# Kernel tuning notes

Measured on AMD Instinct MI355X. Metric: run time of the kernel, lower is better.

## Reference

```python
import jax, jax.numpy as jnp
import numpy as np

B, T, DM = 2, 2048, 1024
H, HKV, DH = 16, 4, 64          # n_heads, n_kv_heads, head_dim
LAT, DFF = 64, 4096             # MLA latent dim, SwiGLU hidden (4*d_model)
SCALE = DH ** -0.5
ROPE_BASE = 10000.0


def _rope(x):
    # x: [B, T, h, DH]; split-half rotary
    half = DH // 2
    pos = jnp.arange(T, dtype=jnp.float32)
    inv_freq = 1.0 / (ROPE_BASE ** (jnp.arange(half, dtype=jnp.float32) / half))
    ang = pos[:, None] * inv_freq                      # [T, half]
    cos = jnp.cos(ang)[None, :, None, :]
    sin = jnp.sin(ang)[None, :, None, :]
    x1, x2 = x[..., :half], x[..., half:]
    return jnp.concatenate([x1 * cos - x2 * sin, x2 * cos + x1 * sin], axis=-1)


def setup_inputs() -> dict:
    key = jax.random.key(0)
    ks = jax.random.split(key, 9)
    init = lambda k, shape, fan: jax.random.normal(k, shape, jnp.float32) * (fan ** -0.5)
    return {
        "x": jax.random.normal(ks[0], (B, T, DM), jnp.float32),
        "Wq": init(ks[1], (DM, DM), DM),
        "Wkv_down": init(ks[2], (DM, LAT), DM),
        "Wk_up": init(ks[3], (LAT, HKV * DH), LAT),
        "Wv_up": init(ks[4], (LAT, HKV * DH), LAT),
        "Wgate": init(ks[5], (DH, DH), DH),
        "bgate": jnp.zeros((DH,), jnp.float32),
        "Wo1": init(ks[6], (DM, DFF), DM),
        "Wo2": init(ks[7], (DFF, DM), DFF),
    }


def reference(x, Wq, Wkv_down, Wk_up, Wv_up, Wgate, bgate, Wo1, Wo2):
    # GQA projections; MLA: shared low-rank latent -> K/V up-projections
    q = (x @ Wq).reshape(B, T, H, DH)
    lat = x @ Wkv_down                                  # [B, T, LAT]
    k = (lat @ Wk_up).reshape(B, T, HKV, DH)
    v = (lat @ Wv_up).reshape(B, T, HKV, DH)

    q = _rope(q)
    k = _rope(k)

    # repeat KV heads (GQA): kv head g serves q heads [g*rep, (g+1)*rep)
    rep = H // HKV
    k = jnp.repeat(k, rep, axis=2)                      # [B, T, H, DH]
    v = jnp.repeat(v, rep, axis=2)

    scores = jnp.einsum("bthd,bshd->bhts", q, k) * SCALE
    causal = jnp.tril(jnp.ones((T, T), dtype=bool))
    scores = jnp.where(causal[None, None], scores, -jnp.inf)
    attn = jax.nn.softmax(scores, axis=-1)
    out = jnp.einsum("bhts,bshd->bthd", attn, v)        # [B, T, H, DH]

    # Gated attention (G1, per_head): sigmoid gate after attention
    gate = jax.nn.sigmoid(out @ Wgate + bgate)
    out = (out * gate).reshape(B, T, DM)

    # SwiGLU-style out_proj: Linear -> SiLU -> Linear
    h = jax.nn.silu(out @ Wo1)
    return h @ Wo2
```

## Files before the change

kernel.cpp:

```cpp
#include <hip/hip_runtime.h>
#include <math.h>

#define NB 2
#define NT 2048
#define NDM 1024
#define NH 16
#define NHKV 4
#define NDH 64
#define NLAT 64
#define NDFF 4096

typedef __attribute__((ext_vector_type(4))) float fx4;
typedef __attribute__((ext_vector_type(8))) short bf8;
typedef __attribute__((ext_vector_type(4))) unsigned short us4;
typedef __attribute__((ext_vector_type(8))) unsigned short us8;

__device__ __forceinline__ unsigned short f2bf(float f) {
  union { float f; unsigned int u; } v; v.f = f;
  unsigned int u = v.u;
  u += 0x7fffu + ((u >> 16) & 1u);
  return (unsigned short)(u >> 16);
}
__device__ __forceinline__ float bf2f(unsigned short h) {
  union { unsigned u; float f; } v; v.u = ((unsigned)h) << 16; return v.f;
}

__global__ void conv_bf_k(const float* __restrict__ in,
                          unsigned short* __restrict__ out, int n8) {
  int idx = blockIdx.x * 256 + threadIdx.x;
  if (idx >= n8) return;
  fx4 a = *(const fx4*)(in + (size_t)idx * 8);
  fx4 b = *(const fx4*)(in + (size_t)idx * 8 + 4);
  us8 o = { f2bf(a[0]), f2bf(a[1]), f2bf(a[2]), f2bf(a[3]),
            f2bf(b[0]), f2bf(b[1]), f2bf(b[2]), f2bf(b[3]) };
  *(us8*)(out + (size_t)idx * 8) = o;
}

__global__ __launch_bounds__(256) void convT_bf_k(const float* __restrict__ W,
                                                  unsigned short* __restrict__ Wt,
                                                  int K, int N) {
  __shared__ float tile[64 * 65];
  const int t = threadIdx.x;
  const int k0 = blockIdx.x * 64, n0 = blockIdx.y * 64;
#pragma unroll
  for (int i = 0; i < 4; ++i) {
    int id = t + 256 * i;
    int row = id >> 4, c = (id & 15) * 4;
    fx4 v = *(const fx4*)(W + (size_t)(k0 + row) * N + n0 + c);
    tile[row * 65 + c + 0] = v[0];
    tile[row * 65 + c + 1] = v[1];
    tile[row * 65 + c + 2] = v[2];
    tile[row * 65 + c + 3] = v[3];
  }
  __syncthreads();
  const int nr = t >> 2, kc = (t & 3) * 16;
  us8 o0, o1;
#pragma unroll
  for (int e = 0; e < 8; ++e) o0[e] = f2bf(tile[(kc + e) * 65 + nr]);
#pragma unroll
  for (int e = 0; e < 8; ++e) o1[e] = f2bf(tile[(kc + 8 + e) * 65 + nr]);
  *(us8*)(Wt + (size_t)(n0 + nr) * K + k0 + kc) = o0;
  *(us8*)(Wt + (size_t)(n0 + nr) * K + k0 + kc + 8) = o1;
}

__device__ __forceinline__ bf8 fragG(const unsigned short* base, int row, int gr) {
  const unsigned short* rb = base + row * 64;
  const int r7 = row & 7;
  us4 lo = *(const us4*)(rb + 8 * ((gr >> 1) ^ r7) + 4 * (gr & 1));
  us4 hi = *(const us4*)(rb + 8 * (((gr + 4) >> 1) ^ r7) + 4 * (gr & 1));
  bf8 f;
  f[0] = (short)lo[0]; f[1] = (short)lo[1]; f[2] = (short)lo[2]; f[3] = (short)lo[3];
  f[4] = (short)hi[0]; f[5] = (short)hi[1]; f[6] = (short)hi[2]; f[7] = (short)hi[3];
  return f;
}

template<int EPI>
__global__ __launch_bounds__(256) void gemm_bf_k(const unsigned short* __restrict__ A,
                                                 const unsigned short* __restrict__ Bt,
                                                 void* __restrict__ Cp,
                                                 int M, int N, int K) {
  __shared__ __align__(16) unsigned short As[128 * 64];
  __shared__ __align__(16) unsigned short Bs[128 * 64];
  const int t = threadIdx.x;
  const int m0 = blockIdx.x * 128, n0 = blockIdx.y * 128;
  const int lane = t & 63, w = t >> 6;
  const int n = lane & 15, g = lane >> 4;
  const int wr = w >> 1, wc = w & 1;
  const int lrow = lane >> 3;
  const int lslot = (lane & 7) ^ lrow;
  const unsigned short* srcA = A  + (size_t)(m0 + 32 * w + lrow) * K + 8 * lslot;
  const unsigned short* srcB = Bt + (size_t)(n0 + 32 * w + lrow) * K + 8 * lslot;
  fx4 acc[4][4];
#pragma unroll
  for (int mt = 0; mt < 4; ++mt)
#pragma unroll
    for (int nt = 0; nt < 4; ++nt) acc[mt][nt] = fx4{0.f, 0.f, 0.f, 0.f};

  for (int k0 = 0; k0 < K; k0 += 64) {
    __syncthreads();
#pragma unroll
    for (int u = 0; u < 4; ++u) {
      __builtin_amdgcn_global_load_lds(
          (const __attribute__((address_space(1))) unsigned int*)(srcA + (size_t)(8 * u) * K + k0),
          (__attribute__((address_space(3))) unsigned int*)(As + (32 * w + 8 * u) * 64),
          16, 0, 0);
      __builtin_amdgcn_global_load_lds(
          (const __attribute__((address_space(1))) unsigned int*)(srcB + (size_t)(8 * u) * K + k0),
          (__attribute__((address_space(3))) unsigned int*)(Bs + (32 * w + 8 * u) * 64),
          16, 0, 0);
    }
    __syncthreads();
#pragma unroll
    for (int ks = 0; ks < 2; ++ks) {
      bf8 af[4], bfr[4];
#pragma unroll
      for (int mt = 0; mt < 4; ++mt)
        af[mt] = fragG(As, wr * 64 + mt * 16 + n, 8 * ks + g);
#pragma unroll
      for (int nt = 0; nt < 4; ++nt)
        bfr[nt] = fragG(Bs, wc * 64 + nt * 16 + n, 8 * ks + g);
#pragma unroll
      for (int mt = 0; mt < 4; ++mt)
#pragma unroll
        for (int nt = 0; nt < 4; ++nt)
          acc[mt][nt] = __builtin_amdgcn_mfma_f32_16x16x32_bf16(af[mt], bfr[nt], acc[mt][nt], 0, 0, 0);
    }
  }
#pragma unroll
  for (int mt = 0; mt < 4; ++mt)
#pragma unroll
    for (int nt = 0; nt < 4; ++nt)
#pragma unroll
      for (int r = 0; r < 4; ++r) {
        int row = m0 + wr * 64 + mt * 16 + 4 * g + r;
        int col = n0 + wc * 64 + nt * 16 + n;
        float v = acc[mt][nt][r];
        if (EPI == 1) {
          float s = v / (1.f + __expf(-v));
          ((unsigned short*)Cp)[(size_t)row * N + col] = f2bf(s);
        } else {
          ((float*)Cp)[(size_t)row * N + col] = v;
        }
      }
}

template<int ABF16, int EPI>
__global__ __launch_bounds__(256) void gemm_k(const void* __restrict__ Ap,
                                              const float* __restrict__ Bp,
                                              void* __restrict__ Cp,
                                              int M, int N, int K) {
  constexpr int LDK = 68;
  __shared__ unsigned short As[64 * LDK];
  __shared__ unsigned short Bs[64 * LDK];
  const int t = threadIdx.x;
  const int m0 = blockIdx.x * 64, n0 = blockIdx.y * 64;
  const int lane = t & 63, w = t >> 6;
  const int m16 = lane & 15, g = lane >> 4;
  const int arow = w * 16 + m16;
  fx4 acc[4] = {{0.f,0.f,0.f,0.f},{0.f,0.f,0.f,0.f},{0.f,0.f,0.f,0.f},{0.f,0.f,0.f,0.f}};

  for (int k0 = 0; k0 < K; k0 += 64) {
    __syncthreads();
#pragma unroll
    for (int i = 0; i < 4; ++i) {
      int id = t * 4 + i;
      int row = id >> 4, cg = (id & 15) * 4;
      if (ABF16) {
        const unsigned short* A = (const unsigned short*)Ap;
        *(us4*)(As + row * LDK + cg) =
            *(const us4*)(A + (size_t)(m0 + row) * K + k0 + cg);
      } else {
        const float* A = (const float*)Ap;
        fx4 a = *(const fx4*)(A + (size_t)(m0 + row) * K + k0 + cg);
        us4 ab = { f2bf(a[0]), f2bf(a[1]), f2bf(a[2]), f2bf(a[3]) };
        *(us4*)(As + row * LDK + cg) = ab;
      }
      fx4 bv = *(const fx4*)(Bp + (size_t)(k0 + row) * N + n0 + cg);
      Bs[(cg + 0) * LDK + row] = f2bf(bv[0]);
      Bs[(cg + 1) * LDK + row] = f2bf(bv[1]);
      Bs[(cg + 2) * LDK + row] = f2bf(bv[2]);
      Bs[(cg + 3) * LDK + row] = f2bf(bv[3]);
    }
    __syncthreads();
#pragma unroll
    for (int ks = 0; ks < 2; ++ks) {
      const int kb = ks * 32;
      us4 a0 = *(const us4*)(As + arow * LDK + kb + 4 * g);
      us4 a1 = *(const us4*)(As + arow * LDK + kb + 16 + 4 * g);
      bf8 af;
      af[0] = (short)a0[0]; af[1] = (short)a0[1]; af[2] = (short)a0[2]; af[3] = (short)a0[3];
      af[4] = (short)a1[0]; af[5] = (short)a1[1]; af[6] = (short)a1[2]; af[7] = (short)a1[3];
#pragma unroll
      for (int nt = 0; nt < 4; ++nt) {
        const int brow = nt * 16 + m16;
        us4 b0 = *(const us4*)(Bs + brow * LDK + kb + 4 * g);
        us4 b1 = *(const us4*)(Bs + brow * LDK + kb + 16 + 4 * g);
        bf8 bf_;
        bf_[0] = (short)b0[0]; bf_[1] = (short)b0[1]; bf_[2] = (short)b0[2]; bf_[3] = (short)b0[3];
        bf_[4] = (short)b1[0]; bf_[5] = (short)b1[1]; bf_[6] = (short)b1[2]; bf_[7] = (short)b1[3];
        acc[nt] = __builtin_amdgcn_mfma_f32_16x16x32_bf16(af, bf_, acc[nt], 0, 0, 0);
      }
    }
  }
#pragma unroll
  for (int nt = 0; nt < 4; ++nt) {
#pragma unroll
    for (int r = 0; r < 4; ++r) {
      int row = m0 + w * 16 + 4 * g + r;
      int col = n0 + nt * 16 + m16;
      float vv = acc[nt][r];
      if (EPI == 1) {
        float s = vv / (1.f + __expf(-vv));
        ((unsigned short*)Cp)[(size_t)row * N + col] = f2bf(s);
      } else {
        ((float*)Cp)[(size_t)row * N + col] = vv;
      }
    }
  }
}

__global__ void rope_k(float* __restrict__ x, int nheads, int total) {
  int idx = blockIdx.x * 256 + threadIdx.x;
  if (idx >= total) return;
  int i = idx & 31;
  int rest = idx >> 5;
  int tpos = (rest / nheads) % NT;
  float* p = x + (size_t)rest * NDH;
  float ang = (float)tpos * powf(10000.0f, -(float)i * (1.0f / 32.0f));
  float sn, cs;
  sincosf(ang, &sn, &cs);
  float x1 = p[i], x2 = p[i + 32];
  p[i]      = x1 * cs - x2 * sn;
  p[i + 32] = x2 * cs + x1 * sn;
}

__device__ __forceinline__ bf8 frag64(const unsigned short* base, int row, int gr) {
  const unsigned short* rb = base + row * 72;
  us4 lo = *(const us4*)(rb + 4 * gr);
  us4 hi = *(const us4*)(rb + 4 * gr + 16);
  bf8 f;
  f[0] = (short)lo[0]; f[1] = (short)lo[1]; f[2] = (short)lo[2]; f[3] = (short)lo[3];
  f[4] = (short)hi[0]; f[5] = (short)hi[1]; f[6] = (short)hi[2]; f[7] = (short)hi[3];
  return f;
}
__device__ __forceinline__ bf8 frag64v(const unsigned short* base, int row, int gr) {
  const unsigned short* rb = base + row * 72 + 8 * ((row >> 3) & 1);
  us4 lo = *(const us4*)(rb + 4 * gr);
  us4 hi = *(const us4*)(rb + 4 * gr + 16);
  bf8 f;
  f[0] = (short)lo[0]; f[1] = (short)lo[1]; f[2] = (short)lo[2]; f[3] = (short)lo[3];
  f[4] = (short)hi[0]; f[5] = (short)hi[1]; f[6] = (short)hi[2]; f[7] = (short)hi[3];
  return f;
}

__global__ __launch_bounds__(256) void attn_mfma_k(const float* __restrict__ qb,
                                                   const float* __restrict__ kb,
                                                   const float* __restrict__ vb,
                                                   const float* __restrict__ Wg,
                                                   const float* __restrict__ bg,
                                                   unsigned short* __restrict__ outp) {
  __shared__ __align__(16) char smem[36352];
  unsigned short* Qs  = (unsigned short*)smem;
  unsigned short* Ks  = Qs + 64 * 72;
  unsigned short* Vt  = Ks + 64 * 72;
  unsigned short* wgs = Vt + 64 * 72;
  float* outs = (float*)smem;

  const int t = threadIdx.x;
  const int q0 = blockIdx.x * 64;
  const int bh = blockIdx.y;
  const int b = bh >> 4, h = bh & 15, kvh = h >> 2;
  const int lane = t & 63, wq = t >> 6;
  const int n = lane & 15, g = lane >> 4;
  const int srow = 4 * wq + g;
  const int c = n;

#pragma unroll
  for (int i = 0; i < 4; ++i) {
    int id = t + 256 * i;
    int row = id >> 4, cc = id & 15;
    fx4 wv = *(const fx4*)(Wg + (size_t)id * 4);
    us4 wb = { f2bf(wv[0]), f2bf(wv[1]), f2bf(wv[2]), f2bf(wv[3]) };
    *(us4*)(wgs + row * 68 + 4 * cc) = wb;
    fx4 a = *(const fx4*)(qb + (((size_t)b * NT + q0 + row) * NH + h) * NDH + 4 * cc);
    us4 ab = { f2bf(a[0]), f2bf(a[1]), f2bf(a[2]), f2bf(a[3]) };
    *(us4*)(Qs + row * 72 + 4 * cc) = ab;
  }
  __syncthreads();

  const int qrow_l = wq * 16 + n;
  bf8 bq0 = frag64(Qs, qrow_l, g);
  bf8 bq1 = frag64(Qs, qrow_l, g + 8);

  float mrun = -INFINITY, lsum = 0.f;
  fx4 oacc[4] = {{0.f,0.f,0.f,0.f},{0.f,0.f,0.f,0.f},{0.f,0.f,0.f,0.f},{0.f,0.f,0.f,0.f}};

  for (int s0 = 0; s0 <= q0; s0 += 64) {
    __syncthreads();
#pragma unroll
    for (int i = 0; i < 4; ++i) {
      const int row = srow + 16 * i;
      const size_t base = (((size_t)b * NT + s0 + row) * NHKV + kvh) * NDH + 4 * c;
      fx4 kv4 = *(const fx4*)(kb + base);
      us4 ab = { f2bf(kv4[0]), f2bf(kv4[1]), f2bf(kv4[2]), f2bf(kv4[3]) };
      *(us4*)(Ks + row * 72 + 4 * c) = ab;

      fx4 vv4 = *(const fx4*)(vb + base);
      float u0 = vv4[0], u1 = vv4[1], u2 = vv4[2], u3 = vv4[3];
      float t0 = __shfl_xor((g & 2) ? u0 : u2, 32);
      float t1 = __shfl_xor((g & 2) ? u1 : u3, 32);
      if (g & 2) { u0 = t0; u1 = t1; } else { u2 = t0; u3 = t1; }
      float s0v = __shfl_xor((g & 1) ? u0 : u1, 16);
      float s1v = __shfl_xor((g & 1) ? u2 : u3, 16);
      if (g & 1) { u0 = s0v; u2 = s1v; } else { u1 = s0v; u3 = s1v; }
      const int dd = 4 * c + g;
      const int r0 = 4 * wq + 16 * i;
      us4 tv = { f2bf(u0), f2bf(u1), f2bf(u2), f2bf(u3) };
      *(us4*)(Vt + dd * 72 + 8 * ((dd >> 3) & 1) + r0) = tv;
    }
    __syncthreads();

    float sc[16];
#pragma unroll
    for (int nt = 0; nt < 4; ++nt) {
      const int krow = 16 * nt + n;
      bf8 ka0 = frag64(Ks, krow, g);
      bf8 ka1 = frag64(Ks, krow, g + 8);
      fx4 s4 = {0.f, 0.f, 0.f, 0.f};
      s4 = __builtin_amdgcn_mfma_f32_16x16x32_bf16(ka0, bq0, s4, 0, 0, 0);
      s4 = __builtin_amdgcn_mfma_f32_16x16x32_bf16(ka1, bq1, s4, 0, 0, 0);
#pragma unroll
      for (int r = 0; r < 4; ++r) sc[nt * 4 + r] = s4[r] * 0.125f;
    }
    if (s0 == q0) {
#pragma unroll
      for (int nt = 0; nt < 4; ++nt)
#pragma unroll
        for (int r = 0; r < 4; ++r)
          if (16 * nt + 4 * g + r > wq * 16 + n) sc[nt * 4 + r] = -INFINITY;
    }

    float tm = sc[0];
#pragma unroll
    for (int i = 1; i < 16; ++i) tm = fmaxf(tm, sc[i]);
    tm = fmaxf(tm, __shfl_xor(tm, 16));
    tm = fmaxf(tm, __shfl_xor(tm, 32));
    float mnew = fmaxf(mrun, tm);
    float corr = __expf(mrun - mnew);
    float p[16];
    float ls = 0.f;
#pragma unroll
    for (int i = 0; i < 16; ++i) { p[i] = __expf(sc[i] - mnew); ls += p[i]; }
    ls += __shfl_xor(ls, 16);
    ls += __shfl_xor(ls, 32);
    lsum = lsum * corr + ls;
    mrun = mnew;
#pragma unroll
    for (int dt = 0; dt < 4; ++dt) oacc[dt] *= corr;

    bf8 pb0, pb1;
#pragma unroll
    for (int j = 0; j < 8; ++j) {
      pb0[j] = (short)f2bf(p[j]);
      pb1[j] = (short)f2bf(p[8 + j]);
    }

#pragma unroll
    for (int dt = 0; dt < 4; ++dt) {
      const int vrow = 16 * dt + n;
      bf8 va0 = frag64v(Vt, vrow, g);
      bf8 va1 = frag64v(Vt, vrow, g + 8);
      oacc[dt] = __builtin_amdgcn_mfma_f32_16x16x32_bf16(va0, pb0, oacc[dt], 0, 0, 0);
      oacc[dt] = __builtin_amdgcn_mfma_f32_16x16x32_bf16(va1, pb1, oacc[dt], 0, 0, 0);
    }
  }

  __syncthreads();
  const float inv = 1.0f / lsum;
#pragma unroll
  for (int dt = 0; dt < 4; ++dt)
#pragma unroll
    for (int r = 0; r < 4; ++r)
      outs[(16 * wq + n) * 68 + 16 * dt + 4 * g + r] = oacc[dt][r] * inv;
  __syncthreads();

  const int r = t >> 2, qd = t & 3;
  fx4 gs[4];
#pragma unroll
  for (int j = 0; j < 4; ++j) gs[j] = *(const fx4*)(bg + qd * 16 + j * 4);
  for (int d = 0; d < 64; ++d) {
    float od = outs[r * 68 + d];
    const unsigned short* wr = wgs + d * 68 + qd * 16;
#pragma unroll
    for (int j = 0; j < 4; ++j) {
      us4 wv = *(const us4*)(wr + j * 4);
      gs[j][0] += bf2f(wv[0]) * od;
      gs[j][1] += bf2f(wv[1]) * od;
      gs[j][2] += bf2f(wv[2]) * od;
      gs[j][3] += bf2f(wv[3]) * od;
    }
  }
  unsigned short* op = outp + ((size_t)b * NT + q0 + r) * NDM + h * NDH + qd * 16;
#pragma unroll
  for (int j = 0; j < 4; ++j) {
    fx4 o = *(const fx4*)(outs + r * 68 + qd * 16 + j * 4);
    us4 rb;
#pragma unroll
    for (int e = 0; e < 4; ++e) {
      float gv = 1.f / (1.f + __expf(-gs[j][e]));
      rb[e] = f2bf(o[e] * gv);
    }
    *(us4*)(op + j * 4) = rb;
  }
}

extern "C" void kernel_launch(void* const* d_in, const int* in_sizes, int n_in,
                              void* d_out, int out_size, void* d_ws, size_t ws_size,
                              hipStream_t stream) {
  const float* x    = (const float*)d_in[0];
  const float* Wq   = (const float*)d_in[1];
  const float* Wkvd = (const float*)d_in[2];
  const float* Wku  = (const float*)d_in[3];
  const float* Wvu  = (const float*)d_in[4];
  const float* Wg   = (const float*)d_in[5];
  const float* bg   = (const float*)d_in[6];
  const float* Wo1  = (const float*)d_in[7];
  const float* Wo2  = (const float*)d_in[8];
  float* out = (float*)d_out;
  char* ws = (char*)d_ws;

  float*          q     = (float*)(ws);
  float*          lat   = (float*)(ws + 16777216);
  float*          kk    = (float*)(ws + 17825792);
  float*          vv    = (float*)(ws + 22020096);
  unsigned short* xb    = (unsigned short*)(ws + 26214400);
  unsigned short* hbuf  = (unsigned short*)(ws);
  unsigned short* WqT   = (unsigned short*)(ws + 34602880);
  unsigned short* Wo1T  = (unsigned short*)(ws + 36700160);
  unsigned short* Wo2T  = (unsigned short*)(ws + 45088768);
  unsigned short* aob   = (unsigned short*)(ws + 53477376);

  const int MT = NB * NT;
  dim3 blk(256);

  conv_bf_k<<<dim3(MT * NDM / 8 / 256), blk, 0, stream>>>(x, xb, MT * NDM / 8);
  convT_bf_k<<<dim3(NDM / 64, NDM / 64),  blk, 0, stream>>>(Wq,  WqT,  NDM, NDM);
  convT_bf_k<<<dim3(NDM / 64, NDFF / 64), blk, 0, stream>>>(Wo1, Wo1T, NDM, NDFF);
  convT_bf_k<<<dim3(NDFF / 64, NDM / 64), blk, 0, stream>>>(Wo2, Wo2T, NDFF, NDM);

  gemm_bf_k<0><<<dim3(MT/128, NDM/128), blk, 0, stream>>>(xb, WqT, (void*)q, MT, NDM, NDM);
  gemm_k<0,0><<<dim3(MT/64, NLAT/64), blk, 0, stream>>>((const void*)x,   Wkvd, (void*)lat, MT, NLAT,      NDM);
  gemm_k<0,0><<<dim3(MT/64, (NHKV*NDH)/64), blk, 0, stream>>>((const void*)lat, Wku, (void*)kk, MT, NHKV*NDH, NLAT);
  gemm_k<0,0><<<dim3(MT/64, (NHKV*NDH)/64), blk, 0, stream>>>((const void*)lat, Wvu, (void*)vv, MT, NHKV*NDH, NLAT);

  int qpairs = NB * NT * NH * 32;
  int kpairs = NB * NT * NHKV * 32;
  rope_k<<<dim3((qpairs + 255) / 256), blk, 0, stream>>>(q,  NH,   qpairs);
  rope_k<<<dim3((kpairs + 255) / 256), blk, 0, stream>>>(kk, NHKV, kpairs);

  attn_mfma_k<<<dim3(NT/64, NB*NH), blk, 0, stream>>>(q, kk, vv, Wg, bg, aob);

  gemm_bf_k<1><<<dim3(MT/128, NDFF/128), blk, 0, stream>>>(aob,  Wo1T, (void*)hbuf, MT, NDFF, NDM);
  gemm_bf_k<0><<<dim3(MT/128, NDM/128),  blk, 0, stream>>>(hbuf, Wo2T, (void*)out,  MT, NDM,  NDFF);
}
```

Measured before the change: 459.0 us.

## Process 128 queries per attention block, balance causal work, swizzle GEMM tiles

Result: faster. 445.3 us (-3.0%).

```diff
diff --git a/kernel.cpp b/kernel.cpp
--- a/kernel.cpp
+++ b/kernel.cpp
@@ -1,4 +1,5 @@
 #include <hip/hip_runtime.h>
+#include <hip/hip_bf16.h>
 #include <math.h>
 
 #define NB 2
@@ -16,10 +17,10 @@
 typedef __attribute__((ext_vector_type(8))) unsigned short us8;
 
 __device__ __forceinline__ unsigned short f2bf(float f) {
-  union { float f; unsigned int u; } v; v.f = f;
-  unsigned int u = v.u;
-  u += 0x7fffu + ((u >> 16) & 1u);
-  return (unsigned short)(u >> 16);
+  __hip_bfloat16 h = __float2bfloat16(f);
+  unsigned short u;
+  __builtin_memcpy(&u, &h, 2);
+  return u;
 }
 __device__ __forceinline__ float bf2f(unsigned short h) {
   union { unsigned u; float f; } v; v.u = ((unsigned)h) << 16; return v.f;
@@ -82,7 +83,12 @@
   __shared__ __align__(16) unsigned short As[128 * 64];
   __shared__ __align__(16) unsigned short Bs[128 * 64];
   const int t = threadIdx.x;
-  const int m0 = blockIdx.x * 128, n0 = blockIdx.y * 128;
+  const int nwg = gridDim.x * gridDim.y;
+  int orig = blockIdx.y * gridDim.x + blockIdx.x;
+  int tileid = orig;
+  if ((nwg & 7) == 0) tileid = (orig & 7) * (nwg >> 3) + (orig >> 3);
+  const int bxg = tileid % gridDim.x, byg = tileid / gridDim.x;
+  const int m0 = bxg * 128, n0 = byg * 128;
   const int lane = t & 63, w = t >> 6;
   const int n = lane & 15, g = lane >> 4;
   const int wr = w >> 1, wc = w & 1;
@@ -253,21 +259,24 @@
   return f;
 }
 
-__global__ __launch_bounds__(256) void attn_mfma_k(const float* __restrict__ qb,
-                                                   const float* __restrict__ kb,
-                                                   const float* __restrict__ vb,
-                                                   const float* __restrict__ Wg,
-                                                   const float* __restrict__ bg,
-                                                   unsigned short* __restrict__ outp) {
-  __shared__ __align__(16) char smem[36352];
+__global__ __launch_bounds__(256) void attn_mfma2_k(const float* __restrict__ qb,
+                                                    const float* __restrict__ kb,
+                                                    const float* __restrict__ vb,
+                                                    const float* __restrict__ Wg,
+                                                    const float* __restrict__ bg,
+                                                    unsigned short* __restrict__ outp) {
+  __shared__ __align__(16) char smem[45568];
   unsigned short* Qs  = (unsigned short*)smem;
-  unsigned short* Ks  = Qs + 64 * 72;
+  unsigned short* Ks  = Qs + 128 * 72;
   unsigned short* Vt  = Ks + 64 * 72;
   unsigned short* wgs = Vt + 64 * 72;
   float* outs = (float*)smem;
 
   const int t = threadIdx.x;
-  const int q0 = blockIdx.x * 64;
+  const int gx = gridDim.x;
+  const int bx = blockIdx.x;
+  const int bxp = (bx & 1) ? (gx - 1 - (bx >> 1)) : (bx >> 1);
+  const int q0 = bxp * 128;
   const int bh = blockIdx.y;
   const int b = bh >> 4, h = bh & 15, kvh = h >> 2;
   const int lane = t & 63, wq = t >> 6;
@@ -282,20 +291,27 @@
     fx4 wv = *(const fx4*)(Wg + (size_t)id * 4);
     us4 wb = { f2bf(wv[0]), f2bf(wv[1]), f2bf(wv[2]), f2bf(wv[3]) };
     *(us4*)(wgs + row * 68 + 4 * cc) = wb;
+  }
+#pragma unroll
+  for (int i = 0; i < 8; ++i) {
+    int id = t + 256 * i;
+    int row = id >> 4, cc = id & 15;
     fx4 a = *(const fx4*)(qb + (((size_t)b * NT + q0 + row) * NH + h) * NDH + 4 * cc);
-    us4 ab = { f2bf(a[0]), f2bf(a[1]), f2bf(a[2]), f2bf(a[3]) };
+    us4 ab = { f2bf(a[0] * 0.125f), f2bf(a[1] * 0.125f),
+               f2bf(a[2] * 0.125f), f2bf(a[3] * 0.125f) };
     *(us4*)(Qs + row * 72 + 4 * cc) = ab;
   }
   __syncthreads();
 
   const int qrow_l = wq * 16 + n;
-  bf8 bq0 = frag64(Qs, qrow_l, g);
-  bf8 bq1 = frag64(Qs, qrow_l, g + 8);
-
-  float mrun = -INFINITY, lsum = 0.f;
-  fx4 oacc[4] = {{0.f,0.f,0.f,0.f},{0.f,0.f,0.f,0.f},{0.f,0.f,0.f,0.f},{0.f,0.f,0.f,0.f}};
-
-  for (int s0 = 0; s0 <= q0; s0 += 64) {
+  bf8 bq00 = frag64(Qs, qrow_l, g),      bq01 = frag64(Qs, qrow_l, g + 8);
+  bf8 bq10 = frag64(Qs, 64 + qrow_l, g), bq11 = frag64(Qs, 64 + qrow_l, g + 8);
+
+  float mrun0 = -INFINITY, lsum0 = 0.f, mrun1 = -INFINITY, lsum1 = 0.f;
+  fx4 oacc0[4] = {{0.f,0.f,0.f,0.f},{0.f,0.f,0.f,0.f},{0.f,0.f,0.f,0.f},{0.f,0.f,0.f,0.f}};
+  fx4 oacc1[4] = {{0.f,0.f,0.f,0.f},{0.f,0.f,0.f,0.f},{0.f,0.f,0.f,0.f},{0.f,0.f,0.f,0.f}};
+
+  for (int s0 = 0; s0 <= q0 + 64; s0 += 64) {
     __syncthreads();
 #pragma unroll
     for (int i = 0; i < 4; ++i) {
@@ -320,97 +336,115 @@
     }
     __syncthreads();
 
-    float sc[16];
-#pragma unroll
-    for (int nt = 0; nt < 4; ++nt) {
-      const int krow = 16 * nt + n;
-      bf8 ka0 = frag64(Ks, krow, g);
-      bf8 ka1 = frag64(Ks, krow, g + 8);
-      fx4 s4 = {0.f, 0.f, 0.f, 0.f};
-      s4 = __builtin_amdgcn_mfma_f32_16x16x32_bf16(ka0, bq0, s4, 0, 0, 0);
-      s4 = __builtin_amdgcn_mfma_f32_16x16x32_bf16(ka1, bq1, s4, 0, 0, 0);
-#pragma unroll
-      for (int r = 0; r < 4; ++r) sc[nt * 4 + r] = s4[r] * 0.125f;
-    }
-    if (s0 == q0) {
-#pragma unroll
-      for (int nt = 0; nt < 4; ++nt)
-#pragma unroll
-        for (int r = 0; r < 4; ++r)
-          if (16 * nt + 4 * g + r > wq * 16 + n) sc[nt * 4 + r] = -INFINITY;
-    }
-
-    float tm = sc[0];
-#pragma unroll
-    for (int i = 1; i < 16; ++i) tm = fmaxf(tm, sc[i]);
-    tm = fmaxf(tm, __shfl_xor(tm, 16));
-    tm = fmaxf(tm, __shfl_xor(tm, 32));
-    float mnew = fmaxf(mrun, tm);
-    float corr = __expf(mrun - mnew);
-    float p[16];
-    float ls = 0.f;
-#pragma unroll
-    for (int i = 0; i < 16; ++i) { p[i] = __expf(sc[i] - mnew); ls += p[i]; }
-    ls += __shfl_xor(ls, 16);
-    ls += __shfl_xor(ls, 32);
-    lsum = lsum * corr + ls;
-    mrun = mnew;
-#pragma unroll
-    for (int dt = 0; dt < 4; ++dt) oacc[dt] *= corr;
-
-    bf8 pb0, pb1;
-#pragma unroll
-    for (int j = 0; j < 8; ++j) {
-      pb0[j] = (short)f2bf(p[j]);
-      pb1[j] = (short)f2bf(p[8 + j]);
-    }
-
-#pragma unroll
-    for (int dt = 0; dt < 4; ++dt) {
-      const int vrow = 16 * dt + n;
-      bf8 va0 = frag64v(Vt, vrow, g);
-      bf8 va1 = frag64v(Vt, vrow, g + 8);
-      oacc[dt] = __builtin_amdgcn_mfma_f32_16x16x32_bf16(va0, pb0, oacc[dt], 0, 0, 0);
-      oacc[dt] = __builtin_amdgcn_mfma_f32_16x16x32_bf16(va1, pb1, oacc[dt], 0, 0, 0);
+    const int hstart = (s0 == q0 + 64) ? 1 : 0;
+#pragma unroll
+    for (int hh = 0; hh < 2; ++hh) {
+      if (hh < hstart) continue;
+      const bf8 bqa = hh ? bq10 : bq00;
+      const bf8 bqb = hh ? bq11 : bq01;
+      float sc[16];
+#pragma unroll
+      for (int nt = 0; nt < 4; ++nt) {
+        const int krow = 16 * nt + n;
+        bf8 ka0 = frag64(Ks, krow, g);
+        bf8 ka1 = frag64(Ks, krow, g + 8);
+        fx4 s4 = {0.f, 0.f, 0.f, 0.f};
+        s4 = __builtin_amdgcn_mfma_f32_16x16x32_bf16(ka0, bqa, s4, 0, 0, 0);
+        s4 = __builtin_amdgcn_mfma_f32_16x16x32_bf16(ka1, bqb, s4, 0, 0, 0);
+#pragma unroll
+        for (int r = 0; r < 4; ++r) sc[nt * 4 + r] = s4[r];
+      }
+      if (s0 == q0 + 64 * hh) {
+#pragma unroll
+        for (int nt = 0; nt < 4; ++nt)
+#pragma unroll
+          for (int r = 0; r < 4; ++r)
+            if (16 * nt + 4 * g + r > qrow_l) sc[nt * 4 + r] = -INFINITY;
+      }
+      float mr = hh ? mrun1 : mrun0;
+      float lz = hh ? lsum1 : lsum0;
+      float tm = sc[0];
+#pragma unroll
+      for (int i = 1; i < 16; ++i) tm = fmaxf(tm, sc[i]);
+      tm = fmaxf(tm, __shfl_xor(tm, 16));
+      tm = fmaxf(tm, __shfl_xor(tm, 32));
+      float mnew = fmaxf(mr, tm);
+      float corr = __expf(mr - mnew);
+      float p[16];
+      float ls = 0.f;
+#pragma unroll
+      for (int i = 0; i < 16; ++i) { p[i] = __expf(sc[i] - mnew); ls += p[i]; }
+      ls += __shfl_xor(ls, 16);
+      ls += __shfl_xor(ls, 32);
+      lz = lz * corr + ls;
+      if (hh) { mrun1 = mnew; lsum1 = lz; } else { mrun0 = mnew; lsum0 = lz; }
+
+      bf8 pb0, pb1;
+#pragma unroll
+      for (int j = 0; j < 8; ++j) {
+        pb0[j] = (short)f2bf(p[j]);
+        pb1[j] = (short)f2bf(p[8 + j]);
+      }
+#pragma unroll
+      for (int dt = 0; dt < 4; ++dt) {
+        const int vrow = 16 * dt + n;
+        bf8 va0 = frag64v(Vt, vrow, g);
+        bf8 va1 = frag64v(Vt, vrow, g + 8);
+        if (hh) {
+          oacc1[dt] *= corr;
+          oacc1[dt] = __builtin_amdgcn_mfma_f32_16x16x32_bf16(va0, pb0, oacc1[dt], 0, 0, 0);
+          oacc1[dt] = __builtin_amdgcn_mfma_f32_16x16x32_bf16(va1, pb1, oacc1[dt], 0, 0, 0);
+        } else {
+          oacc0[dt] *= corr;
+          oacc0[dt] = __builtin_amdgcn_mfma_f32_16x16x32_bf16(va0, pb0, oacc0[dt], 0, 0, 0);
+          oacc0[dt] = __builtin_amdgcn_mfma_f32_16x16x32_bf16(va1, pb1, oacc0[dt], 0, 0, 0);
+        }
+      }
     }
   }
 
   __syncthreads();
-  const float inv = 1.0f / lsum;
+  const float inv0 = 1.0f / lsum0, inv1 = 1.0f / lsum1;
 #pragma unroll
   for (int dt = 0; dt < 4; ++dt)
 #pragma unroll
-    for (int r = 0; r < 4; ++r)
-      outs[(16 * wq + n) * 68 + 16 * dt + 4 * g + r] = oacc[dt][r] * inv;
+    for (int r = 0; r < 4; ++r) {
+      outs[(qrow_l) * 68 + 16 * dt + 4 * g + r]      = oacc0[dt][r] * inv0;
+      outs[(64 + qrow_l) * 68 + 16 * dt + 4 * g + r] = oacc1[dt][r] * inv1;
+    }
   __syncthreads();
 
   const int r = t >> 2, qd = t & 3;
-  fx4 gs[4];
-#pragma unroll
-  for (int j = 0; j < 4; ++j) gs[j] = *(const fx4*)(bg + qd * 16 + j * 4);
-  for (int d = 0; d < 64; ++d) {
-    float od = outs[r * 68 + d];
-    const unsigned short* wr = wgs + d * 68 + qd * 16;
+#pragma unroll
+  for (int ih = 0; ih < 2; ++ih) {
+    const int rr = 64 * ih + r;
+    fx4 gs[4];
+#pragma unroll
+    for (int j = 0; j < 4; ++j) gs[j] = *(const fx4*)(bg + qd * 16 + j * 4);
+    for (int d = 0; d < 64; ++d) {
+      float od = outs[rr * 68 + d];
+      const unsigned short* wr = wgs + d * 68 + qd * 16;
+#pragma unroll
+      for (int j = 0; j < 4; ++j) {
+        us4 wv = *(const us4*)(wr + j * 4);
+        gs[j][0] += bf2f(wv[0]) * od;
+        gs[j][1] += bf2f(wv[1]) * od;
+        gs[j][2] += bf2f(wv[2]) * od;
+        gs[j][3] += bf2f(wv[3]) * od;
+      }
+    }
+    unsigned short* op = outp + ((size_t)b * NT + q0 + rr) * NDM + h * NDH + qd * 16;
 #pragma unroll
     for (int j = 0; j < 4; ++j) {
-      us4 wv = *(const us4*)(wr + j * 4);
-      gs[j][0] += bf2f(wv[0]) * od;
-      gs[j][1] += bf2f(wv[1]) * od;
-      gs[j][2] += bf2f(wv[2]) * od;
-      gs[j][3] += bf2f(wv[3]) * od;
-    }
-  }
-  unsigned short* op = outp + ((size_t)b * NT + q0 + r) * NDM + h * NDH + qd * 16;
-#pragma unroll
-  for (int j = 0; j < 4; ++j) {
-    fx4 o = *(const fx4*)(outs + r * 68 + qd * 16 + j * 4);
-    us4 rb;
-#pragma unroll
-    for (int e = 0; e < 4; ++e) {
-      float gv = 1.f / (1.f + __expf(-gs[j][e]));
-      rb[e] = f2bf(o[e] * gv);
-    }
-    *(us4*)(op + j * 4) = rb;
+      fx4 o = *(const fx4*)(outs + rr * 68 + qd * 16 + j * 4);
+      us4 rbv;
+#pragma unroll
+      for (int e = 0; e < 4; ++e) {
+        float gv = 1.f / (1.f + __expf(-gs[j][e]));
+        rbv[e] = f2bf(o[e] * gv);
+      }
+      *(us4*)(op + j * 4) = rbv;
+    }
   }
 }
 
@@ -458,7 +492,7 @@
   rope_k<<<dim3((qpairs + 255) / 256), blk, 0, stream>>>(q,  NH,   qpairs);
   rope_k<<<dim3((kpairs + 255) / 256), blk, 0, stream>>>(kk, NHKV, kpairs);
 
-  attn_mfma_k<<<dim3(NT/64, NB*NH), blk, 0, stream>>>(q, kk, vv, Wg, bg, aob);
+  attn_mfma2_k<<<dim3(NT/128, NB*NH), blk, 0, stream>>>(q, kk, vv, Wg, bg, aob);
 
   gemm_bf_k<1><<<dim3(MT/128, NDFF/128), blk, 0, stream>>>(aob,  Wo1T, (void*)hbuf, MT, NDFF, NDM);
   gemm_bf_k<0><<<dim3(MT/128, NDM/128),  blk, 0, stream>>>(hbuf, Wo2T, (void*)out,  MT, NDM,  NDFF);
```
